# Optimization experiments

Hardware: AMD Instinct MI355X
Metric: run time of the kernel (lower is better)

## Reference

```python
import jax, jax.numpy as jnp
import numpy as np

D = 256   # model dim
M = 64    # num mechanisms
B = 4
S = 8192


def setup_inputs() -> dict:
    key = jax.random.key(0)
    ks = jax.random.split(key, 16)
    n = jax.random.normal
    inp = {
        "x": n(ks[0], (B, S, D), jnp.float32),
        "context": n(ks[1], (B, S, D), jnp.float32),
        # stacked per-mechanism params (m, out, in) etc.
        "Wm": n(ks[2], (M, D, D), jnp.float32) * (1.0 / np.sqrt(D)),
        "bm": n(ks[3], (M, D), jnp.float32) * 0.02,
        "cm": n(ks[4], (M, D), jnp.float32),           # characteristics (1,1,dim) per node
        "um": n(ks[5], (M, D), jnp.float32) * (1.0 / np.sqrt(D)),  # timing_gate weight
        "vm": n(ks[6], (M,), jnp.float32) * 0.02,       # timing_gate bias
        # selector: Linear(d, 2d) -> GELU -> Linear(2d, m)
        "W1": n(ks[7], (2 * D, D), jnp.float32) * (1.0 / np.sqrt(D)),
        "b1": n(ks[8], (2 * D,), jnp.float32) * 0.02,
        "W2": n(ks[9], (M, 2 * D), jnp.float32) * (1.0 / np.sqrt(2 * D)),
        "b2": n(ks[10], (M,), jnp.float32) * 0.02,
        # integrate: Linear(2d, d)
        "Wi": n(ks[11], (D, 2 * D), jnp.float32) * (1.0 / np.sqrt(2 * D)),
        "bi": n(ks[12], (D,), jnp.float32) * 0.02,
    }
    return inp


def reference(x, context, Wm, bm, cm, um, vm, W1, b1, W2, b2, Wi, bi):
    # selector: softmax over mechanisms (b, s, m)
    h = jax.nn.gelu(jnp.einsum('bsd,ed->bse', context, W1) + b1, approximate=False)
    scores = jax.nn.softmax(jnp.einsum('bse,me->bsm', h, W2) + b2, axis=-1)

    # per-mechanism sigmoid timing gate (b, s, m)
    gate = jax.nn.sigmoid(jnp.einsum('bsd,md->bsm', x, um) + vm)

    # combined weight a[b,s,m] = softmax_score * gate; then
    # selected = sum_m a * (x @ Wm.T + bm + cm)  -- contracted without
    # materializing the (b, s, m, d) stack the torch loop builds.
    a = scores * gate                               # (b, s, m)
    selected = jnp.einsum('bsm,bse,mde->bsd', a, x, Wm) \
             + jnp.einsum('bsm,md->bsd', a, bm + cm)

    # integrate(concat([x, selected]))
    cat = jnp.concatenate([x, selected], axis=-1)   # (b, s, 2d)
    integrated = jnp.einsum('bse,de->bsd', cat, Wi) + bi
    return integrated
```

## Files before the change

### kernel.cpp

```cpp
#include <hip/hip_runtime.h>
#include <cstdint>
#include <cstddef>


typedef _Float16 f16;
typedef f16 f16x8 __attribute__((ext_vector_type(8)));
typedef float f32x4 __attribute__((ext_vector_type(4)));

#define DEV __device__ __forceinline__

DEV uint32_t swz128(uint32_t b) { return b ^ (((b >> 7) & 7u) << 4); }
DEV uint32_t swz512(uint32_t b) { return b ^ (((b >> 9) & 7u) << 4); }

DEV void gload_lds16(const void* g, void* l) {
  __builtin_amdgcn_global_load_lds(
      (const __attribute__((address_space(1))) unsigned int*)g,
      (__attribute__((address_space(3))) unsigned int*)l, 16, 0, 0);
}

DEV f16x8 cvt8(float4 u0, float4 u1) {
  f16x8 v = {(f16)u0.x, (f16)u0.y, (f16)u0.z, (f16)u0.w,
             (f16)u1.x, (f16)u1.y, (f16)u1.z, (f16)u1.w};
  return v;
}

__global__ void prep_b_kernel(const float* __restrict__ S, f16* __restrict__ dst,
                              int K, int BN, int total) {
  int t = blockIdx.x * 256 + threadIdx.x;
  if (t >= total) return;
  int gpc = BN * 8;
  int g = t % gpc;
  int c = (t / gpc) % (K / 64);
  int cb = t / (gpc * (K / 64));
  int ks = g / (BN * 4);
  int rem = g % (BN * 4);
  int col = rem >> 2;
  int kg = rem & 3;
  int J = cb * BN + col;
  int k = c * 64 + ks * 32 + kg * 8;
  const float* s = S + (size_t)J * K + k;
  float4 u0 = *(const float4*)s;
  float4 u1 = *(const float4*)(s + 4);
  f16* chunk = dst + (size_t)(cb * (K / 64) + c) * (BN * 64);
  *(f16x8*)((char*)chunk + swz128((uint32_t)g * 16)) = cvt8(u0, u1);
}

__global__ void prep_wcat_kernel(const float* __restrict__ Wm,
                                 const float* __restrict__ bm,
                                 const float* __restrict__ cm,
                                 f16* __restrict__ dst) {
  int t = blockIdx.x * 256 + threadIdx.x;
  if (t >= 257 * 2048) return;
  int g = t & 2047;
  int c = t >> 11;
  int ks = g >> 10;
  int rem = g & 1023;
  int col = rem >> 2;
  int kg = rem & 3;
  int k0 = ks * 32 + kg * 8;
  f16x8 v;
  if (c < 256) {
    int m = c & 63;
    int e0 = (c >> 6) * 64 + k0;
    const float* s = Wm + ((size_t)m * 256 + col) * 256 + e0;
    float4 u0 = *(const float4*)s;
    float4 u1 = *(const float4*)(s + 4);
    v = cvt8(u0, u1);
  } else {
#pragma unroll
    for (int j = 0; j < 8; ++j) {
      int k = k0 + j;
      v[j] = (f16)(bm[k * 256 + col] + cm[k * 256 + col]);
    }
  }
  *(f16x8*)((char*)(dst + (size_t)c * 16384) + swz128((uint32_t)g * 16)) = v;
}

template <int BN, int NCHUNK, int A0C, int EPI>
__global__ __launch_bounds__(BN == 256 ? 512 : 256, 2)
void gemm_tpl(const float* __restrict__ A0, int lda0,
              const f16* __restrict__ A1, int lda1,
              const f16* __restrict__ Bt,
              const float* __restrict__ bias,
              float* __restrict__ outF, f16* __restrict__ outH, int ldo) {
  constexpr int WAVES = (BN == 256) ? 8 : 4;
  constexpr int THREADS = WAVES * 64;
  constexpr int WC = (BN == 256) ? 4 : 1;
  constexpr int WR = WAVES / WC;
  constexpr int RT = 128 / (WR * 16);
  constexpr int CT = (BN / WC) / 16;

  __shared__ alignas(16) f16 sA[2][128 * 64];
  __shared__ alignas(16) f16 sB[2][BN * 64];

  const int tid = threadIdx.x;
  const int lane = tid & 63;
  const int wid = tid >> 6;
  const int wr = wid / WC, wc = wid % WC;
  const int rb = blockIdx.x, cb = blockIdx.y;

  auto stageB = [&](int c, int buf) {
    const char* src = (const char*)(Bt + (size_t)(cb * NCHUNK + c) * (BN * 64));
#pragma unroll
    for (int it = 0; it < (BN * 64 * 2) / (THREADS * 16); ++it) {
      int off = (it * THREADS + tid) * 16;
      gload_lds16(src + off, (char*)&sB[buf][0] + off);
    }
  };
  auto stageA = [&](int c, int buf) {
#pragma unroll
    for (int it = 0; it < 1024 / THREADS; ++it) {
      int gg = it * THREADS + tid;
      int row = gg >> 3, eg = gg & 7;
      size_t rowG = (size_t)rb * 128 + row;
      f16x8 v;
      if (A0C > 0 && c < A0C) {
        const float* s = A0 + rowG * lda0 + c * 64 + eg * 8;
        float4 u0 = *(const float4*)s;
        float4 u1 = *(const float4*)(s + 4);
        v = cvt8(u0, u1);
      } else {
        v = *(const f16x8*)(A1 + rowG * lda1 + (c - A0C) * 64 + eg * 8);
      }
      *(f16x8*)((char*)&sA[buf][0] + swz128((uint32_t)(row * 128 + eg * 16))) = v;
    }
  };

  f32x4 acc[RT][CT];
#pragma unroll
  for (int i = 0; i < RT; ++i)
#pragma unroll
    for (int j = 0; j < CT; ++j) acc[i][j] = (f32x4){0.f, 0.f, 0.f, 0.f};

  stageB(0, 0);
  stageA(0, 0);
  __syncthreads();

  for (int c = 0; c < NCHUNK; ++c) {
    int cur = c & 1;
    if (c + 1 < NCHUNK) {
      stageB(c + 1, cur ^ 1);
      stageA(c + 1, cur ^ 1);
    }
#pragma unroll
    for (int ks = 0; ks < 2; ++ks) {
      f16x8 af[RT], bf[CT];
#pragma unroll
      for (int rt = 0; rt < RT; ++rt) {
        int row = wr * (RT * 16) + rt * 16 + (lane & 15);
        af[rt] = *(const f16x8*)((const char*)&sA[cur][0] +
                                 swz128((uint32_t)(row * 128 + ks * 64 + (lane >> 4) * 16)));
      }
#pragma unroll
      for (int ct = 0; ct < CT; ++ct) {
        int col = wc * (CT * 16) + ct * 16 + (lane & 15);
        bf[ct] = *(const f16x8*)((const char*)&sB[cur][0] +
                                 swz128((uint32_t)(((ks * BN + col) * 4 + (lane >> 4)) * 16)));
      }
#pragma unroll
      for (int rt = 0; rt < RT; ++rt)
#pragma unroll
        for (int ct = 0; ct < CT; ++ct)
          acc[rt][ct] = __builtin_amdgcn_mfma_f32_16x16x32_f16(af[rt], bf[ct], acc[rt][ct], 0, 0, 0);
    }
    __syncthreads();
  }

#pragma unroll
  for (int rt = 0; rt < RT; ++rt)
#pragma unroll
    for (int ct = 0; ct < CT; ++ct)
#pragma unroll
      for (int i = 0; i < 4; ++i) {
        size_t row = (size_t)rb * 128 + wr * (RT * 16) + rt * 16 + (lane >> 4) * 4 + i;
        int colG = cb * BN + wc * (CT * 16) + ct * 16 + (lane & 15);
        float v = acc[rt][ct][i];
        if constexpr (EPI == 0) {
          if (bias) v += bias[colG];
          outF[row * ldo + colG] = v;
        } else {
          v += bias[colG];
          float ge = 0.5f * v * (1.0f + erff(v * 0.70710678118f));
          outH[row * ldo + colG] = (f16)ge;
        }
      }
}

__global__ void selector_finish(const float* __restrict__ logits,
                                const float* __restrict__ glog,
                                const float* __restrict__ b2,
                                const float* __restrict__ vm,
                                f16* __restrict__ a16) {
  int n = blockIdx.x * 4 + (threadIdx.x >> 6);
  int m = threadIdx.x & 63;
  float l = logits[(size_t)n * 64 + m] + b2[m];
  float mx = l;
#pragma unroll
  for (int o = 32; o; o >>= 1) mx = fmaxf(mx, __shfl_xor(mx, o));
  float p = expf(l - mx);
  float s = p;
#pragma unroll
  for (int o = 32; o; o >>= 1) s += __shfl_xor(s, o);
  float g = glog[(size_t)n * 64 + m] + vm[m];
  float gate = 1.0f / (1.0f + expf(-g));
  a16[(size_t)n * 64 + m] = (f16)(p / s * gate);
}

__global__ __launch_bounds__(512, 2)
void big_gemm(const float* __restrict__ x, const f16* __restrict__ a16,
              const f16* __restrict__ Wcat, f16* __restrict__ sel) {
  __shared__ alignas(16) f16 sX[128 * 256];
  __shared__ alignas(16) f16 sAa[128 * 72];
  __shared__ alignas(16) f16 sB[2][256 * 64];

  const int tid = threadIdx.x;
  const int lane = tid & 63;
  const int wid = tid >> 6;
  const int wr = wid >> 2, wc = wid & 3;
  const int rb = blockIdx.x;

  auto stageB = [&](int c, int buf) {
    const char* src = (const char*)(Wcat + (size_t)c * 16384);
#pragma unroll
    for (int it = 0; it < 4; ++it) {
      int off = (it * 512 + tid) * 16;
      gload_lds16(src + off, (char*)&sB[buf][0] + off);
    }
  };

#pragma unroll
  for (int it = 0; it < 8; ++it) {
    int gg = it * 512 + tid;
    int row = gg >> 5, eg = gg & 31;
    const float* s = x + ((size_t)rb * 128 + row) * 256 + eg * 8;
    float4 u0 = *(const float4*)s;
    float4 u1 = *(const float4*)(s + 4);
    *(f16x8*)((char*)sX + swz512((uint32_t)(row * 512 + eg * 16))) = cvt8(u0, u1);
  }
#pragma unroll
  for (int it = 0; it < 2; ++it) {
    int gg = it * 512 + tid;
    int row = gg >> 3, mg = gg & 7;
    f16x8 v = *(const f16x8*)(a16 + ((size_t)rb * 128 + row) * 64 + mg * 8);
    *(f16x8*)((char*)sAa + row * 144 + mg * 16) = v;
  }
  stageB(0, 0);
  asm volatile("s_waitcnt vmcnt(0) lgkmcnt(0)" ::: "memory");
  __builtin_amdgcn_s_barrier();

  f32x4 acc[4][4];
#pragma unroll
  for (int i = 0; i < 4; ++i)
#pragma unroll
    for (int j = 0; j < 4; ++j) acc[i][j] = (f32x4){0.f, 0.f, 0.f, 0.f};

  const int row0 = wr * 64 + (lane & 15);
  f16x8 xv[2][4];

  for (int q = 0; q < 256; ++q) {
    int cur = q & 1;
    stageB(q + 1, cur ^ 1);
    asm volatile("s_waitcnt vmcnt(4)" ::: "memory");
    __builtin_amdgcn_s_barrier();

    if ((q & 63) == 0) {
      int ebyte = (q >> 6) * 128;
#pragma unroll
      for (int ks = 0; ks < 2; ++ks)
#pragma unroll
        for (int rt = 0; rt < 4; ++rt) {
          int row = row0 + rt * 16;
          xv[ks][rt] = *(const f16x8*)((const char*)sX +
              swz512((uint32_t)(row * 512 + ebyte + ks * 64 + (lane >> 4) * 16)));
        }
    }
    int m = q & 63;
    f16 as[4];
#pragma unroll
    for (int rt = 0; rt < 4; ++rt) as[rt] = sAa[(row0 + rt * 16) * 72 + m];

#pragma unroll
    for (int ks = 0; ks < 2; ++ks) {
      f16x8 bf[4];
#pragma unroll
      for (int ct = 0; ct < 4; ++ct) {
        int col = wc * 64 + ct * 16 + (lane & 15);
        bf[ct] = *(const f16x8*)((const char*)&sB[cur][0] +
                   swz128((uint32_t)(((ks * 256 + col) * 4 + (lane >> 4)) * 16)));
      }
      f16x8 af[4];
#pragma unroll
      for (int rt = 0; rt < 4; ++rt) af[rt] = xv[ks][rt] * as[rt];
      __builtin_amdgcn_s_setprio(1);
#pragma unroll
      for (int rt = 0; rt < 4; ++rt)
#pragma unroll
        for (int ct = 0; ct < 4; ++ct)
          acc[rt][ct] = __builtin_amdgcn_mfma_f32_16x16x32_f16(af[rt], bf[ct], acc[rt][ct], 0, 0, 0);
      __builtin_amdgcn_s_setprio(0);
    }
    __builtin_amdgcn_sched_barrier(0);
    __builtin_amdgcn_s_barrier();
  }

  asm volatile("s_waitcnt vmcnt(0)" ::: "memory");
  __builtin_amdgcn_s_barrier();
#pragma unroll
  for (int ks = 0; ks < 2; ++ks) {
    f16x8 af[4], bf[4];
#pragma unroll
    for (int rt = 0; rt < 4; ++rt) {
      int row = row0 + rt * 16;
      af[rt] = *(const f16x8*)((const char*)sAa + row * 144 + ks * 64 + (lane >> 4) * 16);
    }
#pragma unroll
    for (int ct = 0; ct < 4; ++ct) {
      int col = wc * 64 + ct * 16 + (lane & 15);
      bf[ct] = *(const f16x8*)((const char*)&sB[0][0] +
                 swz128((uint32_t)(((ks * 256 + col) * 4 + (lane >> 4)) * 16)));
    }
#pragma unroll
    for (int rt = 0; rt < 4; ++rt)
#pragma unroll
      for (int ct = 0; ct < 4; ++ct)
        acc[rt][ct] = __builtin_amdgcn_mfma_f32_16x16x32_f16(af[rt], bf[ct], acc[rt][ct], 0, 0, 0);
  }

#pragma unroll
  for (int rt = 0; rt < 4; ++rt)
#pragma unroll
    for (int ct = 0; ct < 4; ++ct)
#pragma unroll
      for (int i = 0; i < 4; ++i) {
        size_t row = (size_t)rb * 128 + wr * 64 + rt * 16 + (lane >> 4) * 4 + i;
        int col = wc * 64 + ct * 16 + (lane & 15);
        sel[row * 256 + col] = (f16)acc[rt][ct][i];
      }
}

extern "C" void kernel_launch(void* const* d_in, const int* in_sizes, int n_in,
                              void* d_out, int out_size, void* d_ws, size_t ws_size,
                              hipStream_t stream) {
  (void)in_sizes; (void)n_in; (void)out_size;
  const float* x   = (const float*)d_in[0];
  const float* ctx = (const float*)d_in[1];
  const float* Wm  = (const float*)d_in[2];
  const float* bm  = (const float*)d_in[3];
  const float* cm  = (const float*)d_in[4];
  const float* um  = (const float*)d_in[5];
  const float* vm  = (const float*)d_in[6];
  const float* W1  = (const float*)d_in[7];
  const float* b1  = (const float*)d_in[8];
  const float* W2  = (const float*)d_in[9];
  const float* b2  = (const float*)d_in[10];
  const float* Wi  = (const float*)d_in[11];
  const float* bi  = (const float*)d_in[12];
  float* out = (float*)d_out;

  char* ws = (char*)d_ws;
  size_t off = 0;
  f16* Wcat = (f16*)(ws + off); off += (size_t)257 * 16384 * 2;
  f16* W1t  = (f16*)(ws + off); off += (size_t)512 * 256 * 2;
  f16* W2t  = (f16*)(ws + off); off += (size_t)64 * 512 * 2;
  f16* umt  = (f16*)(ws + off); off += (size_t)64 * 256 * 2;
  f16* Wit  = (f16*)(ws + off); off += (size_t)256 * 512 * 2;
  f16* h16  = (f16*)(ws + off); off += (size_t)32768 * 512 * 2;
  float* logits = (float*)(ws + off); off += (size_t)32768 * 64 * 4;
  float* glog   = (float*)(ws + off); off += (size_t)32768 * 64 * 4;
  f16* a16   = (f16*)(ws + off); off += (size_t)32768 * 64 * 2;
  f16* sel16 = (f16*)(ws + off); off += (size_t)32768 * 256 * 2;
  if (ws_size < off) return;

  prep_wcat_kernel<<<dim3(257 * 2048 / 256), dim3(256), 0, stream>>>(Wm, bm, cm, Wcat);
  prep_b_kernel<<<dim3(16384 / 256), dim3(256), 0, stream>>>(W1, W1t, 256, 256, 16384);
  prep_b_kernel<<<dim3(4096 / 256),  dim3(256), 0, stream>>>(W2, W2t, 512, 64, 4096);
  prep_b_kernel<<<dim3(2048 / 256),  dim3(256), 0, stream>>>(um, umt, 256, 64, 2048);
  prep_b_kernel<<<dim3(16384 / 256), dim3(256), 0, stream>>>(Wi, Wit, 512, 256, 16384);

  gemm_tpl<256, 4, 4, 1><<<dim3(256, 2), dim3(512), 0, stream>>>(
      ctx, 256, nullptr, 0, W1t, b1, nullptr, h16, 512);
  gemm_tpl<64, 4, 4, 0><<<dim3(256, 1), dim3(256), 0, stream>>>(
      x, 256, nullptr, 0, umt, nullptr, glog, nullptr, 64);
  gemm_tpl<64, 8, 0, 0><<<dim3(256, 1), dim3(256), 0, stream>>>(
      nullptr, 0, h16, 512, W2t, nullptr, logits, nullptr, 64);
  selector_finish<<<dim3(32768 / 4), dim3(256), 0, stream>>>(logits, glog, b2, vm, a16);

  big_gemm<<<dim3(256), dim3(512), 0, stream>>>(x, a16, Wcat, sel16);

  gemm_tpl<256, 8, 4, 0><<<dim3(256, 1), dim3(512), 0, stream>>>(
      x, 256, sel16, 256, Wit, bi, out, nullptr, 256);
}
```

Measured before the change: 398.1 us.

## Deepen B-stage pipeline to four buffers and read x directly into registers

The big GEMM drops the shared-memory copy of x and instead loads and converts x rows straight into registers every 64 steps. The freed LDS is used to quad-buffer Wcat chunks with a prefetch distance of three, so each step needs only one barrier instead of two. The per-step scalar reads of a are replaced by one vector load covering eight steps. The workspace is enlarged so the trailing prefetches stay in bounds. In exchange, the global loads of x now sit inside the loop and add to vmcnt tracking, and the final chunk-256 bias step relies on vmcnt(8) and on buffer 0 holding that chunk, which looks fragile.

```diff
diff --git a/kernel.cpp b/kernel.cpp
--- a/kernel.cpp
+++ b/kernel.cpp
@@ -10,7 +10,6 @@
 #define DEV __device__ __forceinline__
 
 DEV uint32_t swz128(uint32_t b) { return b ^ (((b >> 7) & 7u) << 4); }
-DEV uint32_t swz512(uint32_t b) { return b ^ (((b >> 9) & 7u) << 4); }
 
 DEV void gload_lds16(const void* g, void* l) {
   __builtin_amdgcn_global_load_lds(
@@ -209,15 +208,16 @@
 __global__ __launch_bounds__(512, 2)
 void big_gemm(const float* __restrict__ x, const f16* __restrict__ a16,
               const f16* __restrict__ Wcat, f16* __restrict__ sel) {
-  __shared__ alignas(16) f16 sX[128 * 256];
+  __shared__ alignas(16) f16 sB[4][256 * 64];
   __shared__ alignas(16) f16 sAa[128 * 72];
-  __shared__ alignas(16) f16 sB[2][256 * 64];
 
   const int tid = threadIdx.x;
   const int lane = tid & 63;
   const int wid = tid >> 6;
   const int wr = wid >> 2, wc = wid & 3;
   const int rb = blockIdx.x;
+  const int row0 = wr * 64 + (lane & 15);
+  const int ksub = lane >> 4;
 
   auto stageB = [&](int c, int buf) {
     const char* src = (const char*)(Wcat + (size_t)c * 16384);
@@ -228,15 +228,6 @@
     }
   };
 
-#pragma unroll
-  for (int it = 0; it < 8; ++it) {
-    int gg = it * 512 + tid;
-    int row = gg >> 5, eg = gg & 31;
-    const float* s = x + ((size_t)rb * 128 + row) * 256 + eg * 8;
-    float4 u0 = *(const float4*)s;
-    float4 u1 = *(const float4*)(s + 4);
-    *(f16x8*)((char*)sX + swz512((uint32_t)(row * 512 + eg * 16))) = cvt8(u0, u1);
-  }
 #pragma unroll
   for (int it = 0; it < 2; ++it) {
     int gg = it * 512 + tid;
@@ -245,7 +236,9 @@
     *(f16x8*)((char*)sAa + row * 144 + mg * 16) = v;
   }
   stageB(0, 0);
-  asm volatile("s_waitcnt vmcnt(0) lgkmcnt(0)" ::: "memory");
+  stageB(1, 1);
+  stageB(2, 2);
+  asm volatile("s_waitcnt lgkmcnt(0)" ::: "memory");
   __builtin_amdgcn_s_barrier();
 
   f32x4 acc[4][4];
@@ -254,70 +247,69 @@
 #pragma unroll
     for (int j = 0; j < 4; ++j) acc[i][j] = (f32x4){0.f, 0.f, 0.f, 0.f};
 
-  const int row0 = wr * 64 + (lane & 15);
   f16x8 xv[2][4];
-
-  for (int q = 0; q < 256; ++q) {
-    int cur = q & 1;
-    stageB(q + 1, cur ^ 1);
-    asm volatile("s_waitcnt vmcnt(4)" ::: "memory");
-    __builtin_amdgcn_s_barrier();
-
-    if ((q & 63) == 0) {
-      int ebyte = (q >> 6) * 128;
-#pragma unroll
-      for (int ks = 0; ks < 2; ++ks)
-#pragma unroll
-        for (int rt = 0; rt < 4; ++rt) {
-          int row = row0 + rt * 16;
-          xv[ks][rt] = *(const f16x8*)((const char*)sX +
-              swz512((uint32_t)(row * 512 + ebyte + ks * 64 + (lane >> 4) * 16)));
+  auto loadXV = [&](int er) {
+#pragma unroll
+    for (int ks = 0; ks < 2; ++ks)
+#pragma unroll
+      for (int rt = 0; rt < 4; ++rt) {
+        const float* s = x + ((size_t)rb * 128 + row0 + rt * 16) * 256
+                           + er * 64 + ks * 32 + ksub * 8;
+        float4 u0 = *(const float4*)s;
+        float4 u1 = *(const float4*)(s + 4);
+        xv[ks][rt] = cvt8(u0, u1);
+      }
+  };
+
+  for (int q8 = 0; q8 < 256; q8 += 8) {
+    if ((q8 & 63) == 0) loadXV(q8 >> 6);
+    f16x8 as8[4];
+#pragma unroll
+    for (int rt = 0; rt < 4; ++rt)
+      as8[rt] = *(const f16x8*)((const char*)sAa + (row0 + rt * 16) * 144 + (q8 & 63) * 2);
+#pragma unroll
+    for (int u = 0; u < 8; ++u) {
+      const int q = q8 + u;
+      asm volatile("s_waitcnt vmcnt(8)" ::: "memory");
+      __builtin_amdgcn_s_barrier();
+      stageB(q + 3, (q + 3) & 3);
+      const char* bbase = (const char*)&sB[q & 3][0];
+#pragma unroll
+      for (int ks = 0; ks < 2; ++ks) {
+        f16x8 bf[4];
+#pragma unroll
+        for (int ct = 0; ct < 4; ++ct) {
+          int col = wc * 64 + ct * 16 + (lane & 15);
+          bf[ct] = *(const f16x8*)(bbase +
+                     swz128((uint32_t)(((ks * 256 + col) * 4 + ksub) * 16)));
         }
-    }
-    int m = q & 63;
-    f16 as[4];
-#pragma unroll
-    for (int rt = 0; rt < 4; ++rt) as[rt] = sAa[(row0 + rt * 16) * 72 + m];
-
-#pragma unroll
-    for (int ks = 0; ks < 2; ++ks) {
-      f16x8 bf[4];
-#pragma unroll
-      for (int ct = 0; ct < 4; ++ct) {
-        int col = wc * 64 + ct * 16 + (lane & 15);
-        bf[ct] = *(const f16x8*)((const char*)&sB[cur][0] +
-                   swz128((uint32_t)(((ks * 256 + col) * 4 + (lane >> 4)) * 16)));
-      }
-      f16x8 af[4];
-#pragma unroll
-      for (int rt = 0; rt < 4; ++rt) af[rt] = xv[ks][rt] * as[rt];
-      __builtin_amdgcn_s_setprio(1);
-#pragma unroll
-      for (int rt = 0; rt < 4; ++rt)
-#pragma unroll
-        for (int ct = 0; ct < 4; ++ct)
-          acc[rt][ct] = __builtin_amdgcn_mfma_f32_16x16x32_f16(af[rt], bf[ct], acc[rt][ct], 0, 0, 0);
-      __builtin_amdgcn_s_setprio(0);
-    }
-    __builtin_amdgcn_sched_barrier(0);
-    __builtin_amdgcn_s_barrier();
-  }
-
-  asm volatile("s_waitcnt vmcnt(0)" ::: "memory");
+        f16x8 af[4];
+#pragma unroll
+        for (int rt = 0; rt < 4; ++rt) af[rt] = xv[ks][rt] * as8[rt][u];
+        __builtin_amdgcn_s_setprio(1);
+#pragma unroll
+        for (int rt = 0; rt < 4; ++rt)
+#pragma unroll
+          for (int ct = 0; ct < 4; ++ct)
+            acc[rt][ct] = __builtin_amdgcn_mfma_f32_16x16x32_f16(af[rt], bf[ct], acc[rt][ct], 0, 0, 0);
+        __builtin_amdgcn_s_setprio(0);
+      }
+    }
+  }
+
+  asm volatile("s_waitcnt vmcnt(8)" ::: "memory");
   __builtin_amdgcn_s_barrier();
 #pragma unroll
   for (int ks = 0; ks < 2; ++ks) {
     f16x8 af[4], bf[4];
 #pragma unroll
-    for (int rt = 0; rt < 4; ++rt) {
-      int row = row0 + rt * 16;
-      af[rt] = *(const f16x8*)((const char*)sAa + row * 144 + ks * 64 + (lane >> 4) * 16);
-    }
+    for (int rt = 0; rt < 4; ++rt)
+      af[rt] = *(const f16x8*)((const char*)sAa + (row0 + rt * 16) * 144 + ks * 64 + ksub * 16);
 #pragma unroll
     for (int ct = 0; ct < 4; ++ct) {
       int col = wc * 64 + ct * 16 + (lane & 15);
       bf[ct] = *(const f16x8*)((const char*)&sB[0][0] +
-                 swz128((uint32_t)(((ks * 256 + col) * 4 + (lane >> 4)) * 16)));
+                 swz128((uint32_t)(((ks * 256 + col) * 4 + ksub) * 16)));
     }
 #pragma unroll
     for (int rt = 0; rt < 4; ++rt)
@@ -359,7 +351,7 @@
 
   char* ws = (char*)d_ws;
   size_t off = 0;
-  f16* Wcat = (f16*)(ws + off); off += (size_t)257 * 16384 * 2;
+  f16* Wcat = (f16*)(ws + off); off += (size_t)260 * 16384 * 2;
   f16* W1t  = (f16*)(ws + off); off += (size_t)512 * 256 * 2;
   f16* W2t  = (f16*)(ws + off); off += (size_t)64 * 512 * 2;
   f16* umt  = (f16*)(ws + off); off += (size_t)64 * 256 * 2;
```

Measured after the change: 344.1 us. 13.6% less time.
